# Optimization experiments

Hardware: AMD Instinct MI355X
Metric: run time of the kernel (lower is better)

Reference implementation:

```python
import jax, jax.numpy as jnp
import numpy as np

D_MODEL = 1024
N_HEADS = 16
D_K = D_MODEL // N_HEADS
B, S = 4, 2048


def setup_inputs() -> dict:
    key = jax.random.key(0)
    ks = jax.random.split(key, 5)
    scale = 1.0 / np.sqrt(D_MODEL)  # ~xavier scale for square matrices
    return {
        "Q": jax.random.normal(ks[0], (B, S, D_MODEL), dtype=jnp.float32),
        "length": jax.random.randint(ks[1], (B,), 1, S, dtype=jnp.int32),
        "Wq": jax.random.normal(ks[2], (D_MODEL, D_MODEL), dtype=jnp.float32) * scale,
        "bq": jnp.zeros((D_MODEL,), dtype=jnp.float32),
        "Wk": jax.random.normal(ks[3], (D_MODEL, D_MODEL), dtype=jnp.float32) * scale,
        "bk": jnp.zeros((D_MODEL,), dtype=jnp.float32),
        "Wv": jax.random.normal(ks[4], (D_MODEL, D_MODEL), dtype=jnp.float32) * scale,
        "bv": jnp.zeros((D_MODEL,), dtype=jnp.float32),
    }


def reference(Q, length, Wq, bq, Wk, bk, Wv, bv):
    b, s, d = Q.shape
    q_a = Q @ Wq + bq                                   # [b, s, d]
    # split heads: [b, h, s, d_k]
    q_s = q_a.reshape(b, s, N_HEADS, D_K).transpose(0, 2, 1, 3)
    k_s = (Q @ Wk + bk).reshape(b, s, N_HEADS, D_K).transpose(0, 2, 1, 3)
    v_s = (Q @ Wv + bv).reshape(b, s, N_HEADS, D_K).transpose(0, 2, 1, 3)

    # unnormalized exp attention with multiplicative key mask (faithful to source)
    scores = jnp.einsum("bhqd,bhkd->bhqk", q_s, k_s) / np.sqrt(D_K)
    scores = jnp.exp(scores)
    key_mask = (jnp.arange(s)[None, :] < length[:, None]).astype(scores.dtype)  # [b, k]
    scores = scores * key_mask[:, None, None, :]        # broadcast over heads, queries
    attn = scores / (jnp.sum(scores, axis=-1, keepdims=True) + 1e-8)
    context = jnp.einsum("bhqk,bhkd->bhqd", attn, v_s)
    context = context.transpose(0, 2, 1, 3).reshape(b, s, d)
    return context, q_a
```

## Files before the change

### kernel.cpp

```cpp
#include <hip/hip_runtime.h>

#define D_MODEL 1024
#define N_HEADS 16
#define D_KH    64
#define BATCH   4
#define SEQ     2048
#define M_TOTAL (BATCH*SEQ)

typedef __attribute__((ext_vector_type(8))) short short8;
typedef __attribute__((ext_vector_type(4))) float f32x4;
typedef __attribute__((ext_vector_type(4))) unsigned short u16x4;
typedef __attribute__((ext_vector_type(2))) unsigned int u32x2;

__device__ __forceinline__ unsigned short f2bf(float f) {
  union { float f; unsigned u; } v; v.f = f;
  unsigned r = v.u + 0x7FFFu + ((v.u >> 16) & 1u);
  return (unsigned short)(r >> 16);
}
__device__ __forceinline__ unsigned fbits(float f) {
  union { float f; unsigned u; } v; v.f = f; return v.u;
}

__global__ __launch_bounds__(256) void cvt_q(const float* __restrict__ Q,
                                             unsigned short* __restrict__ Qbf) {
  size_t i = (size_t)blockIdx.x * 256 + threadIdx.x;
  float4 v = ((const float4*)Q)[i];
  u16x4 o;
  o[0] = f2bf(v.x); o[1] = f2bf(v.y); o[2] = f2bf(v.z); o[3] = f2bf(v.w);
  ((u16x4*)Qbf)[i] = o;
}

__global__ __launch_bounds__(256) void cvt_wt(const float* __restrict__ Wq,
                                              const float* __restrict__ Wk,
                                              const float* __restrict__ Wv,
                                              unsigned short* __restrict__ WT) {
  const int z = blockIdx.z;
  const float* W = (z == 0) ? Wq : (z == 1) ? Wk : Wv;
  __shared__ float tile[32][33];
  const int k0 = blockIdx.y * 32, n0 = blockIdx.x * 32;
  const int tx = threadIdx.x & 31, ty = threadIdx.x >> 5;
  for (int i = 0; i < 4; ++i)
    tile[ty + i * 8][tx] = W[(size_t)(k0 + ty + i * 8) * D_MODEL + n0 + tx];
  __syncthreads();
  unsigned short* out = WT + (size_t)z * D_MODEL * D_MODEL;
  for (int i = 0; i < 4; ++i)
    out[(size_t)(n0 + ty + i * 8) * D_MODEL + k0 + tx] = f2bf(tile[tx][ty + i * 8]);
}

#define GQ_BM 128
#define GQ_BN 128
#define GQ_BK 64
#define GQ_NT (D_MODEL / GQ_BK)

__global__ __launch_bounds__(256, 2) void gemm_qkv(
    const unsigned short* __restrict__ Qbf,
    const unsigned short* __restrict__ WT,
    const float* __restrict__ bq_p, const float* __restrict__ bk_p,
    const float* __restrict__ bv_p,
    float* __restrict__ out_qa,
    unsigned short* __restrict__ kbf,
    unsigned short* __restrict__ vt) {
  const int f   = blockIdx.x;
  const int swz = (f & 7) * 192 + (f >> 3);
  const int mm  = swz / 24;
  const int nn  = swz % 24;
  const int m0  = mm * GQ_BM;
  const int n0g = nn * GQ_BN;
  const int z   = n0g >> 10;
  const int n0  = n0g & 1023;

  __shared__ unsigned short smA[2][GQ_BM * GQ_BK];
  __shared__ unsigned short smB[2][GQ_BN * GQ_BK];

  const int t    = threadIdx.x;
  const int lane = t & 63;
  const int w    = t >> 6;
  const int quad = lane >> 4;
  const int l16  = lane & 15;
  const int wr   = w >> 1, wc = w & 1;

  f32x4 acc[4][4];
  for (int i = 0; i < 4; ++i)
    for (int j = 0; j < 4; ++j) acc[i][j] = (f32x4){0.f, 0.f, 0.f, 0.f};

  auto stage = [&](int p, int kt) {
    #pragma unroll
    for (int r = 0; r < 4; ++r) {
      int o   = (r * 256 + t) * 8;
      int row = o >> 6;
      int col = (o & 63) ^ ((row & 7) << 3);
      const unsigned short* ga = Qbf + (size_t)(m0 + row)  * D_MODEL + kt * 64 + col;
      const unsigned short* gb = WT  + (size_t)(n0g + row) * D_MODEL + kt * 64 + col;
      __builtin_amdgcn_global_load_lds(
          (const __attribute__((address_space(1))) void*)ga,
          (__attribute__((address_space(3))) void*)&smA[p][o], 16, 0, 0);
      __builtin_amdgcn_global_load_lds(
          (const __attribute__((address_space(1))) void*)gb,
          (__attribute__((address_space(3))) void*)&smB[p][o], 16, 0, 0);
    }
  };

  stage(0, 0);
  stage(1, 1);
  asm volatile("s_waitcnt vmcnt(8)" ::: "memory");
  __builtin_amdgcn_s_barrier();
  asm volatile("" ::: "memory");

  for (int kt = 0; kt < GQ_NT; ++kt) {
    const int p = kt & 1;

    short8 af[4][2], bf[4][2];
    #pragma unroll
    for (int mi = 0; mi < 4; ++mi) {
      int row = wr * 64 + mi * 16 + l16;
      #pragma unroll
      for (int kk = 0; kk < 2; ++kk)
        af[mi][kk] = *(const short8*)
            &smA[p][(row * 64 + kk * 32 + quad * 8) ^ ((row & 7) << 3)];
    }
    #pragma unroll
    for (int ni = 0; ni < 4; ++ni) {
      int row = wc * 64 + ni * 16 + l16;
      #pragma unroll
      for (int kk = 0; kk < 2; ++kk)
        bf[ni][kk] = *(const short8*)
            &smB[p][(row * 64 + kk * 32 + quad * 8) ^ ((row & 7) << 3)];
    }

    __builtin_amdgcn_s_setprio(1);
    #pragma unroll
    for (int mi = 0; mi < 4; ++mi)
      #pragma unroll
      for (int ni = 0; ni < 4; ++ni) {
        acc[mi][ni] = __builtin_amdgcn_mfma_f32_16x16x32_bf16(
            af[mi][0], bf[ni][0], acc[mi][ni], 0, 0, 0);
        acc[mi][ni] = __builtin_amdgcn_mfma_f32_16x16x32_bf16(
            af[mi][1], bf[ni][1], acc[mi][ni], 0, 0, 0);
      }
    __builtin_amdgcn_s_setprio(0);

    __builtin_amdgcn_s_barrier();
    asm volatile("" ::: "memory");
    if (kt + 2 < GQ_NT) {
      stage(p, kt + 2);
      asm volatile("s_waitcnt vmcnt(8)" ::: "memory");
    } else {
      asm volatile("s_waitcnt vmcnt(0)" ::: "memory");
    }
    __builtin_amdgcn_s_barrier();
    asm volatile("" ::: "memory");
  }

  const float* bias = (z == 0) ? bq_p : (z == 1) ? bk_p : bv_p;
  if (z == 2) {
    for (int ni = 0; ni < 4; ++ni) {
      int n = n0 + wc * 64 + ni * 16 + l16;
      float bval = bias[n];
      int h = n >> 6, d = n & 63;
      for (int mi = 0; mi < 4; ++mi) {
        int m = m0 + wr * 64 + mi * 16 + quad * 4;
        int b = m >> 11, s = m & 2047;
        u16x4 o;
        for (int j = 0; j < 4; ++j) o[j] = f2bf(acc[mi][ni][j] + bval);
        *(u16x4*)&vt[(size_t)((b * 16 + h) * 64 + d) * SEQ + s] = o;
      }
    }
  } else {
    for (int ni = 0; ni < 4; ++ni) {
      int n = n0 + wc * 64 + ni * 16 + l16;
      float bval = bias[n];
      for (int mi = 0; mi < 4; ++mi) {
        int mbase = m0 + wr * 64 + mi * 16 + quad * 4;
        for (int j = 0; j < 4; ++j) {
          float v = acc[mi][ni][j] + bval;
          size_t idx = (size_t)(mbase + j) * D_MODEL + n;
          if (z == 0) out_qa[idx] = v;
          else        kbf[idx] = f2bf(v);
        }
      }
    }
  }
}

#define PST 72
#define QBLK 128

__global__ __launch_bounds__(256, 4) void attn(
    const float* __restrict__ qa,
    const unsigned short* __restrict__ kbf,
    const unsigned short* __restrict__ vt,
    const int* __restrict__ length,
    float* __restrict__ ctx) {
  const int flat = blockIdx.y * 16 + blockIdx.x;
  const int low = flat & 3;
  const int mid = (flat >> 2) & 15;
  const int hi  = flat >> 6;
  const int b  = (low + mid + (mid >> 2) + hi + (hi >> 2)) & 3;
  const int h  = mid;
  const int qt = hi;
  const int bh = b * 16 + h;
  const int len = length[b];

  const int t    = threadIdx.x;
  const int lane = t & 63;
  const int w    = t >> 6;
  const int quad = lane >> 4;
  const int l16  = lane & 15;
  const int r8   = t >> 3;
  const int c8   = (t & 7) * 8;

  __shared__ unsigned short sQ[QBLK * PST];
  __shared__ unsigned short sK[64 * PST];
  __shared__ unsigned short sVT[64 * PST];
  unsigned short* const sP = sQ;

  const float SCL = 0.125f * 1.44269504f;

  for (int half = 0; half < 4; ++half) {
    int r = r8 + half * 32;
    const float* src = qa + (size_t)(b * SEQ + qt * QBLK + r) * D_MODEL + h * D_KH + c8;
    float4 v0 = *(const float4*)src;
    float4 v1 = *(const float4*)(src + 4);
    short8 o;
    o[0] = (short)f2bf(v0.x * SCL); o[1] = (short)f2bf(v0.y * SCL);
    o[2] = (short)f2bf(v0.z * SCL); o[3] = (short)f2bf(v0.w * SCL);
    o[4] = (short)f2bf(v1.x * SCL); o[5] = (short)f2bf(v1.y * SCL);
    o[6] = (short)f2bf(v1.z * SCL); o[7] = (short)f2bf(v1.w * SCL);
    *(short8*)&sQ[r * PST + c8] = o;
  }
  __syncthreads();

  short8 qf00 = *(const short8*)&sQ[(w * 16 + l16) * PST + quad * 8];
  short8 qf01 = *(const short8*)&sQ[(w * 16 + l16) * PST + 32 + quad * 8];
  short8 qf10 = *(const short8*)&sQ[(64 + w * 16 + l16) * PST + quad * 8];
  short8 qf11 = *(const short8*)&sQ[(64 + w * 16 + l16) * PST + 32 + quad * 8];

  f32x4 acc0[4], acc1[4];
  for (int i = 0; i < 4; ++i) {
    acc0[i] = (f32x4){0.f, 0.f, 0.f, 0.f};
    acc1[i] = (f32x4){0.f, 0.f, 0.f, 0.f};
  }
  float den0 = 0.f, den1 = 0.f;

  const unsigned short* kbase_p = kbf + (size_t)b * SEQ * D_MODEL + h * D_KH;
  const unsigned short* vbase_p = vt + (size_t)bh * 64 * SEQ;

  const int nkt = (len + 63) >> 6;

  short8 rk[2], rv[2];
  for (int half = 0; half < 2; ++half) {
    int r = r8 + half * 32;
    rk[half] = *(const short8*)(kbase_p + (size_t)r * D_MODEL + c8);
    rv[half] = *(const short8*)(vbase_p + (size_t)r * SEQ + c8);
  }

  for (int kt = 0; kt < nkt; ++kt) {
    __syncthreads();
    for (int half = 0; half < 2; ++half) {
      int r = r8 + half * 32;
      *(short8*)&sK[r * PST + c8]  = rk[half];
      *(short8*)&sVT[r * PST + c8] = rv[half];
    }
    __syncthreads();

    if (kt + 1 < nkt) {
      for (int half = 0; half < 2; ++half) {
        int r = r8 + half * 32;
        rk[half] = *(const short8*)(kbase_p + (size_t)((kt + 1) * 64 + r) * D_MODEL + c8);
        rv[half] = *(const short8*)(vbase_p + (size_t)r * SEQ + (kt + 1) * 64 + c8);
      }
    }

    const bool full = ((kt + 1) << 6) <= len;

    for (int n = 0; n < 4; ++n) {
      short8 kf0 = *(const short8*)&sK[(n * 16 + l16) * PST + quad * 8];
      short8 kf1 = *(const short8*)&sK[(n * 16 + l16) * PST + 32 + quad * 8];
      f32x4 s0 = (f32x4){0.f, 0.f, 0.f, 0.f};
      s0 = __builtin_amdgcn_mfma_f32_16x16x32_bf16(kf0, qf00, s0, 0, 0, 0);
      s0 = __builtin_amdgcn_mfma_f32_16x16x32_bf16(kf1, qf01, s0, 0, 0, 0);
      f32x4 s1 = (f32x4){0.f, 0.f, 0.f, 0.f};
      s1 = __builtin_amdgcn_mfma_f32_16x16x32_bf16(kf0, qf10, s1, 0, 0, 0);
      s1 = __builtin_amdgcn_mfma_f32_16x16x32_bf16(kf1, qf11, s1, 0, 0, 0);

      float e0, e1, e2, e3, f0, f1, f2, f3;
      if (full) {
        e0 = exp2f(s0[0]); e1 = exp2f(s0[1]); e2 = exp2f(s0[2]); e3 = exp2f(s0[3]);
        f0 = exp2f(s1[0]); f1 = exp2f(s1[1]); f2 = exp2f(s1[2]); f3 = exp2f(s1[3]);
      } else {
        int kb = kt * 64 + n * 16 + quad * 4;
        e0 = (kb + 0 < len) ? exp2f(s0[0]) : 0.f;
        e1 = (kb + 1 < len) ? exp2f(s0[1]) : 0.f;
        e2 = (kb + 2 < len) ? exp2f(s0[2]) : 0.f;
        e3 = (kb + 3 < len) ? exp2f(s0[3]) : 0.f;
        f0 = (kb + 0 < len) ? exp2f(s1[0]) : 0.f;
        f1 = (kb + 1 < len) ? exp2f(s1[1]) : 0.f;
        f2 = (kb + 2 < len) ? exp2f(s1[2]) : 0.f;
        f3 = (kb + 3 < len) ? exp2f(s1[3]) : 0.f;
      }
      den0 += (e0 + e1) + (e2 + e3);
      den1 += (f0 + f1) + (f2 + f3);
      u32x2 pk;
      pk[0] = __builtin_amdgcn_perm(fbits(e1), fbits(e0), 0x07060302);
      pk[1] = __builtin_amdgcn_perm(fbits(e3), fbits(e2), 0x07060302);
      *(u32x2*)&sP[(w * 16 + l16) * PST + n * 16 + quad * 4] = pk;
      u32x2 pk1;
      pk1[0] = __builtin_amdgcn_perm(fbits(f1), fbits(f0), 0x07060302);
      pk1[1] = __builtin_amdgcn_perm(fbits(f3), fbits(f2), 0x07060302);
      *(u32x2*)&sP[(64 + w * 16 + l16) * PST + n * 16 + quad * 4] = pk1;
    }

    short8 pf00 = *(const short8*)&sP[(w * 16 + l16) * PST + quad * 8];
    short8 pf01 = *(const short8*)&sP[(w * 16 + l16) * PST + 32 + quad * 8];
    short8 pf10 = *(const short8*)&sP[(64 + w * 16 + l16) * PST + quad * 8];
    short8 pf11 = *(const short8*)&sP[(64 + w * 16 + l16) * PST + 32 + quad * 8];
    for (int n2 = 0; n2 < 4; ++n2) {
      short8 vf0 = *(const short8*)&sVT[(n2 * 16 + l16) * PST + quad * 8];
      short8 vf1 = *(const short8*)&sVT[(n2 * 16 + l16) * PST + 32 + quad * 8];
      acc0[n2] = __builtin_amdgcn_mfma_f32_16x16x32_bf16(vf0, pf00, acc0[n2], 0, 0, 0);
      acc0[n2] = __builtin_amdgcn_mfma_f32_16x16x32_bf16(vf1, pf01, acc0[n2], 0, 0, 0);
      acc1[n2] = __builtin_amdgcn_mfma_f32_16x16x32_bf16(vf0, pf10, acc1[n2], 0, 0, 0);
      acc1[n2] = __builtin_amdgcn_mfma_f32_16x16x32_bf16(vf1, pf11, acc1[n2], 0, 0, 0);
    }
  }

  den0 += __shfl_xor(den0, 16, 64);
  den0 += __shfl_xor(den0, 32, 64);
  den1 += __shfl_xor(den1, 16, 64);
  den1 += __shfl_xor(den1, 32, 64);
  float inv0 = 1.f / (den0 + 1e-8f);
  float inv1 = 1.f / (den1 + 1e-8f);

  {
    int q0 = qt * QBLK + w * 16 + l16;
    float* dst0 = ctx + (size_t)(b * SEQ + q0) * D_MODEL + h * D_KH;
    float* dst1 = dst0 + (size_t)64 * D_MODEL;
    for (int n2 = 0; n2 < 4; ++n2) {
      f32x4 o0 = acc0[n2];
      f32x4 o1 = acc1[n2];
      *(float4*)(dst0 + n2 * 16 + quad * 4) =
          make_float4(o0[0] * inv0, o0[1] * inv0, o0[2] * inv0, o0[3] * inv0);
      *(float4*)(dst1 + n2 * 16 + quad * 4) =
          make_float4(o1[0] * inv1, o1[1] * inv1, o1[2] * inv1, o1[3] * inv1);
    }
  }
}

extern "C" void kernel_launch(void* const* d_in, const int* in_sizes, int n_in,
                              void* d_out, int out_size, void* d_ws, size_t ws_size,
                              hipStream_t stream) {
  const float* Q      = (const float*)d_in[0];
  const int*   length = (const int*)d_in[1];
  const float* Wq     = (const float*)d_in[2];
  const float* bq     = (const float*)d_in[3];
  const float* Wk     = (const float*)d_in[4];
  const float* bk     = (const float*)d_in[5];
  const float* Wv     = (const float*)d_in[6];
  const float* bv     = (const float*)d_in[7];

  float* out_ctx = (float*)d_out;
  float* out_qa  = out_ctx + (size_t)M_TOTAL * D_MODEL;

  char* ws = (char*)d_ws;
  unsigned short* Qbf = (unsigned short*)ws;
  unsigned short* WT  = (unsigned short*)(ws + (size_t)16 * 1024 * 1024);
  unsigned short* Kbf = (unsigned short*)(ws + (size_t)22 * 1024 * 1024);
  unsigned short* Vt  = (unsigned short*)(ws + (size_t)38 * 1024 * 1024);

  hipLaunchKernelGGL(cvt_q, dim3((M_TOTAL * D_MODEL) / (256 * 4)), dim3(256), 0, stream,
                     Q, Qbf);
  hipLaunchKernelGGL(cvt_wt, dim3(32, 32, 3), dim3(256), 0, stream, Wq, Wk, Wv, WT);
  hipLaunchKernelGGL(gemm_qkv, dim3(64 * 24), dim3(256), 0, stream,
                     Qbf, WT, bq, bk, bv, out_qa, Kbf, Vt);
  hipLaunchKernelGGL(attn, dim3(SEQ / QBLK, BATCH * N_HEADS), dim3(256), 0, stream,
                     out_qa, Kbf, Vt, length, out_ctx);
}
```

Baseline: 243.5 us.

## Split attention key tiles across two wave sets and swizzle shared memory

The attention kernel now launches 512 threads per block. Two groups of four waves each process alternating 64-key tiles for the same 128 queries, and their partial accumulators and denominators are merged through shared memory at the end. The padded LDS layout (stride 72) is replaced by an XOR-swizzled 64-wide layout to avoid bank conflicts. The aim is more waves per block to hide latency and to shorten the serial key loop. In exchange it uses 64KB of LDS, which can lower the number of resident blocks per CU, and adds a reduction step.

```diff
diff --git a/kernel.cpp b/kernel.cpp
--- a/kernel.cpp
+++ b/kernel.cpp
@@ -19,6 +19,9 @@
 }
 __device__ __forceinline__ unsigned fbits(float f) {
   union { float f; unsigned u; } v; v.f = f; return v.u;
+}
+__device__ __forceinline__ int sw(int row, int col) {
+  return row * 64 + (col ^ ((row & 7) << 3));
 }
 
 __global__ __launch_bounds__(256) void cvt_q(const float* __restrict__ Q,
@@ -182,10 +185,9 @@
   }
 }
 
-#define PST 72
 #define QBLK 128
 
-__global__ __launch_bounds__(256, 4) void attn(
+__global__ __launch_bounds__(512, 4) void attn(
     const float* __restrict__ qa,
     const unsigned short* __restrict__ kbf,
     const unsigned short* __restrict__ vt,
@@ -203,22 +205,29 @@
 
   const int t    = threadIdx.x;
   const int lane = t & 63;
-  const int w    = t >> 6;
+  const int wv   = t >> 6;
+  const int set  = wv >> 2;
+  const int w2   = wv & 3;
   const int quad = lane >> 4;
   const int l16  = lane & 15;
-  const int r8   = t >> 3;
-  const int c8   = (t & 7) * 8;
-
-  __shared__ unsigned short sQ[QBLK * PST];
-  __shared__ unsigned short sK[64 * PST];
-  __shared__ unsigned short sVT[64 * PST];
-  unsigned short* const sP = sQ;
+  const int ts   = t & 255;
+  const int rs   = ts >> 3;
+  const int cs   = (ts & 7) * 8;
+
+  __shared__ unsigned char smem[65536];
+  unsigned short* sQP0 = (unsigned short*)smem;
+  unsigned short* sP1  = (unsigned short*)(smem + 16384);
+  unsigned short* sKs  = (unsigned short*)(smem + 32768 + set * 16384);
+  unsigned short* sVTs = sKs + 4096;
+  unsigned short* sPs  = set ? sP1 : sQP0;
+  float* sAcc = (float*)(smem + 32768);
+  float* sDen = (float*)(smem + 16384);
 
   const float SCL = 0.125f * 1.44269504f;
 
-  for (int half = 0; half < 4; ++half) {
-    int r = r8 + half * 32;
-    const float* src = qa + (size_t)(b * SEQ + qt * QBLK + r) * D_MODEL + h * D_KH + c8;
+  for (int half = 0; half < 2; ++half) {
+    int r = (t >> 3) + half * 64;
+    const float* src = qa + (size_t)(b * SEQ + qt * QBLK + r) * D_MODEL + h * D_KH + (t & 7) * 8;
     float4 v0 = *(const float4*)src;
     float4 v1 = *(const float4*)(src + 4);
     short8 o;
@@ -226,14 +235,16 @@
     o[2] = (short)f2bf(v0.z * SCL); o[3] = (short)f2bf(v0.w * SCL);
     o[4] = (short)f2bf(v1.x * SCL); o[5] = (short)f2bf(v1.y * SCL);
     o[6] = (short)f2bf(v1.z * SCL); o[7] = (short)f2bf(v1.w * SCL);
-    *(short8*)&sQ[r * PST + c8] = o;
+    *(short8*)&sQP0[sw(r, (t & 7) * 8)] = o;
   }
   __syncthreads();
 
-  short8 qf00 = *(const short8*)&sQ[(w * 16 + l16) * PST + quad * 8];
-  short8 qf01 = *(const short8*)&sQ[(w * 16 + l16) * PST + 32 + quad * 8];
-  short8 qf10 = *(const short8*)&sQ[(64 + w * 16 + l16) * PST + quad * 8];
-  short8 qf11 = *(const short8*)&sQ[(64 + w * 16 + l16) * PST + 32 + quad * 8];
+  const int qr0 = w2 * 16 + l16;
+  const int qr1 = 64 + qr0;
+  short8 qf00 = *(const short8*)&sQP0[sw(qr0, quad * 8)];
+  short8 qf01 = *(const short8*)&sQP0[sw(qr0, 32 + quad * 8)];
+  short8 qf10 = *(const short8*)&sQP0[sw(qr1, quad * 8)];
+  short8 qf11 = *(const short8*)&sQP0[sw(qr1, 32 + quad * 8)];
 
   f32x4 acc0[4], acc1[4];
   for (int i = 0; i < 4; ++i) {
@@ -245,82 +256,90 @@
   const unsigned short* kbase_p = kbf + (size_t)b * SEQ * D_MODEL + h * D_KH;
   const unsigned short* vbase_p = vt + (size_t)bh * 64 * SEQ;
 
-  const int nkt = (len + 63) >> 6;
+  const int nkt   = (len + 63) >> 6;
+  const int niter = (nkt + 1) >> 1;
 
   short8 rk[2], rv[2];
   for (int half = 0; half < 2; ++half) {
-    int r = r8 + half * 32;
-    rk[half] = *(const short8*)(kbase_p + (size_t)r * D_MODEL + c8);
-    rv[half] = *(const short8*)(vbase_p + (size_t)r * SEQ + c8);
-  }
-
-  for (int kt = 0; kt < nkt; ++kt) {
+    int r = rs + half * 32;
+    rk[half] = *(const short8*)(kbase_p + (size_t)(set * 64 + r) * D_MODEL + cs);
+    rv[half] = *(const short8*)(vbase_p + (size_t)r * SEQ + set * 64 + cs);
+  }
+
+  for (int i = 0; i < niter; ++i) {
+    const int kt = 2 * i + set;
+    const bool active = kt < nkt;
+
     __syncthreads();
-    for (int half = 0; half < 2; ++half) {
-      int r = r8 + half * 32;
-      *(short8*)&sK[r * PST + c8]  = rk[half];
-      *(short8*)&sVT[r * PST + c8] = rv[half];
+    if (active) {
+      for (int half = 0; half < 2; ++half) {
+        int r = rs + half * 32;
+        *(short8*)&sKs[sw(r, cs)]  = rk[half];
+        *(short8*)&sVTs[sw(r, cs)] = rv[half];
+      }
     }
     __syncthreads();
 
-    if (kt + 1 < nkt) {
+    if (kt + 2 < nkt) {
       for (int half = 0; half < 2; ++half) {
-        int r = r8 + half * 32;
-        rk[half] = *(const short8*)(kbase_p + (size_t)((kt + 1) * 64 + r) * D_MODEL + c8);
-        rv[half] = *(const short8*)(vbase_p + (size_t)r * SEQ + (kt + 1) * 64 + c8);
-      }
-    }
-
-    const bool full = ((kt + 1) << 6) <= len;
-
-    for (int n = 0; n < 4; ++n) {
-      short8 kf0 = *(const short8*)&sK[(n * 16 + l16) * PST + quad * 8];
-      short8 kf1 = *(const short8*)&sK[(n * 16 + l16) * PST + 32 + quad * 8];
-      f32x4 s0 = (f32x4){0.f, 0.f, 0.f, 0.f};
-      s0 = __builtin_amdgcn_mfma_f32_16x16x32_bf16(kf0, qf00, s0, 0, 0, 0);
-      s0 = __builtin_amdgcn_mfma_f32_16x16x32_bf16(kf1, qf01, s0, 0, 0, 0);
-      f32x4 s1 = (f32x4){0.f, 0.f, 0.f, 0.f};
-      s1 = __builtin_amdgcn_mfma_f32_16x16x32_bf16(kf0, qf10, s1, 0, 0, 0);
-      s1 = __builtin_amdgcn_mfma_f32_16x16x32_bf16(kf1, qf11, s1, 0, 0, 0);
-
-      float e0, e1, e2, e3, f0, f1, f2, f3;
-      if (full) {
-        e0 = exp2f(s0[0]); e1 = exp2f(s0[1]); e2 = exp2f(s0[2]); e3 = exp2f(s0[3]);
-        f0 = exp2f(s1[0]); f1 = exp2f(s1[1]); f2 = exp2f(s1[2]); f3 = exp2f(s1[3]);
-      } else {
-        int kb = kt * 64 + n * 16 + quad * 4;
-        e0 = (kb + 0 < len) ? exp2f(s0[0]) : 0.f;
-        e1 = (kb + 1 < len) ? exp2f(s0[1]) : 0.f;
-        e2 = (kb + 2 < len) ? exp2f(s0[2]) : 0.f;
-        e3 = (kb + 3 < len) ? exp2f(s0[3]) : 0.f;
-        f0 = (kb + 0 < len) ? exp2f(s1[0]) : 0.f;
-        f1 = (kb + 1 < len) ? exp2f(s1[1]) : 0.f;
-        f2 = (kb + 2 < len) ? exp2f(s1[2]) : 0.f;
-        f3 = (kb + 3 < len) ? exp2f(s1[3]) : 0.f;
-      }
-      den0 += (e0 + e1) + (e2 + e3);
-      den1 += (f0 + f1) + (f2 + f3);
-      u32x2 pk;
-      pk[0] = __builtin_amdgcn_perm(fbits(e1), fbits(e0), 0x07060302);
-      pk[1] = __builtin_amdgcn_perm(fbits(e3), fbits(e2), 0x07060302);
-      *(u32x2*)&sP[(w * 16 + l16) * PST + n * 16 + quad * 4] = pk;
-      u32x2 pk1;
-      pk1[0] = __builtin_amdgcn_perm(fbits(f1), fbits(f0), 0x07060302);
-      pk1[1] = __builtin_amdgcn_perm(fbits(f3), fbits(f2), 0x07060302);
-      *(u32x2*)&sP[(64 + w * 16 + l16) * PST + n * 16 + quad * 4] = pk1;
-    }
-
-    short8 pf00 = *(const short8*)&sP[(w * 16 + l16) * PST + quad * 8];
-    short8 pf01 = *(const short8*)&sP[(w * 16 + l16) * PST + 32 + quad * 8];
-    short8 pf10 = *(const short8*)&sP[(64 + w * 16 + l16) * PST + quad * 8];
-    short8 pf11 = *(const short8*)&sP[(64 + w * 16 + l16) * PST + 32 + quad * 8];
-    for (int n2 = 0; n2 < 4; ++n2) {
-      short8 vf0 = *(const short8*)&sVT[(n2 * 16 + l16) * PST + quad * 8];
-      short8 vf1 = *(const short8*)&sVT[(n2 * 16 + l16) * PST + 32 + quad * 8];
-      acc0[n2] = __builtin_amdgcn_mfma_f32_16x16x32_bf16(vf0, pf00, acc0[n2], 0, 0, 0);
-      acc0[n2] = __builtin_amdgcn_mfma_f32_16x16x32_bf16(vf1, pf01, acc0[n2], 0, 0, 0);
-      acc1[n2] = __builtin_amdgcn_mfma_f32_16x16x32_bf16(vf0, pf10, acc1[n2], 0, 0, 0);
-      acc1[n2] = __builtin_amdgcn_mfma_f32_16x16x32_bf16(vf1, pf11, acc1[n2], 0, 0, 0);
+        int r = rs + half * 32;
+        rk[half] = *(const short8*)(kbase_p + (size_t)((kt + 2) * 64 + r) * D_MODEL + cs);
+        rv[half] = *(const short8*)(vbase_p + (size_t)r * SEQ + (kt + 2) * 64 + cs);
+      }
+    }
+
+    if (active) {
+      const bool full = ((kt + 1) << 6) <= len;
+
+      for (int n = 0; n < 4; ++n) {
+        short8 kf0 = *(const short8*)&sKs[sw(n * 16 + l16, quad * 8)];
+        short8 kf1 = *(const short8*)&sKs[sw(n * 16 + l16, 32 + quad * 8)];
+        f32x4 s0 = (f32x4){0.f, 0.f, 0.f, 0.f};
+        s0 = __builtin_amdgcn_mfma_f32_16x16x32_bf16(kf0, qf00, s0, 0, 0, 0);
+        s0 = __builtin_amdgcn_mfma_f32_16x16x32_bf16(kf1, qf01, s0, 0, 0, 0);
+        f32x4 s1 = (f32x4){0.f, 0.f, 0.f, 0.f};
+        s1 = __builtin_amdgcn_mfma_f32_16x16x32_bf16(kf0, qf10, s1, 0, 0, 0);
+        s1 = __builtin_amdgcn_mfma_f32_16x16x32_bf16(kf1, qf11, s1, 0, 0, 0);
+
+        float e0, e1, e2, e3, f0, f1, f2, f3;
+        if (full) {
+          e0 = exp2f(s0[0]); e1 = exp2f(s0[1]); e2 = exp2f(s0[2]); e3 = exp2f(s0[3]);
+          f0 = exp2f(s1[0]); f1 = exp2f(s1[1]); f2 = exp2f(s1[2]); f3 = exp2f(s1[3]);
+        } else {
+          int kb = kt * 64 + n * 16 + quad * 4;
+          e0 = (kb + 0 < len) ? exp2f(s0[0]) : 0.f;
+          e1 = (kb + 1 < len) ? exp2f(s0[1]) : 0.f;
+          e2 = (kb + 2 < len) ? exp2f(s0[2]) : 0.f;
+          e3 = (kb + 3 < len) ? exp2f(s0[3]) : 0.f;
+          f0 = (kb + 0 < len) ? exp2f(s1[0]) : 0.f;
+          f1 = (kb + 1 < len) ? exp2f(s1[1]) : 0.f;
+          f2 = (kb + 2 < len) ? exp2f(s1[2]) : 0.f;
+          f3 = (kb + 3 < len) ? exp2f(s1[3]) : 0.f;
+        }
+        den0 += (e0 + e1) + (e2 + e3);
+        den1 += (f0 + f1) + (f2 + f3);
+        u32x2 pk;
+        pk[0] = __builtin_amdgcn_perm(fbits(e1), fbits(e0), 0x07060302);
+        pk[1] = __builtin_amdgcn_perm(fbits(e3), fbits(e2), 0x07060302);
+        *(u32x2*)&sPs[sw(qr0, n * 16 + quad * 4)] = pk;
+        u32x2 pk1;
+        pk1[0] = __builtin_amdgcn_perm(fbits(f1), fbits(f0), 0x07060302);
+        pk1[1] = __builtin_amdgcn_perm(fbits(f3), fbits(f2), 0x07060302);
+        *(u32x2*)&sPs[sw(qr1, n * 16 + quad * 4)] = pk1;
+      }
+
+      short8 pf00 = *(const short8*)&sPs[sw(qr0, quad * 8)];
+      short8 pf01 = *(const short8*)&sPs[sw(qr0, 32 + quad * 8)];
+      short8 pf10 = *(const short8*)&sPs[sw(qr1, quad * 8)];
+      short8 pf11 = *(const short8*)&sPs[sw(qr1, 32 + quad * 8)];
+      for (int n2 = 0; n2 < 4; ++n2) {
+        short8 vf0 = *(const short8*)&sVTs[sw(n2 * 16 + l16, quad * 8)];
+        short8 vf1 = *(const short8*)&sVTs[sw(n2 * 16 + l16, 32 + quad * 8)];
+        acc0[n2] = __builtin_amdgcn_mfma_f32_16x16x32_bf16(vf0, pf00, acc0[n2], 0, 0, 0);
+        acc0[n2] = __builtin_amdgcn_mfma_f32_16x16x32_bf16(vf1, pf01, acc0[n2], 0, 0, 0);
+        acc1[n2] = __builtin_amdgcn_mfma_f32_16x16x32_bf16(vf0, pf10, acc1[n2], 0, 0, 0);
+        acc1[n2] = __builtin_amdgcn_mfma_f32_16x16x32_bf16(vf1, pf11, acc1[n2], 0, 0, 0);
+      }
     }
   }
 
@@ -328,20 +347,34 @@
   den0 += __shfl_xor(den0, 32, 64);
   den1 += __shfl_xor(den1, 16, 64);
   den1 += __shfl_xor(den1, 32, 64);
-  float inv0 = 1.f / (den0 + 1e-8f);
-  float inv1 = 1.f / (den1 + 1e-8f);
-
-  {
-    int q0 = qt * QBLK + w * 16 + l16;
-    float* dst0 = ctx + (size_t)(b * SEQ + q0) * D_MODEL + h * D_KH;
-    float* dst1 = dst0 + (size_t)64 * D_MODEL;
+
+  __syncthreads();
+  if (set == 1) {
+    #pragma unroll
     for (int n2 = 0; n2 < 4; ++n2) {
-      f32x4 o0 = acc0[n2];
-      f32x4 o1 = acc1[n2];
-      *(float4*)(dst0 + n2 * 16 + quad * 4) =
-          make_float4(o0[0] * inv0, o0[1] * inv0, o0[2] * inv0, o0[3] * inv0);
-      *(float4*)(dst1 + n2 * 16 + quad * 4) =
-          make_float4(o1[0] * inv1, o1[1] * inv1, o1[2] * inv1, o1[3] * inv1);
+      int col = n2 * 16 + quad * 4;
+      *(f32x4*)&sAcc[qr0 * 64 + (col ^ ((qr0 & 7) << 2))] = acc0[n2];
+      *(f32x4*)&sAcc[qr1 * 64 + (col ^ ((qr1 & 7) << 2))] = acc1[n2];
+    }
+    if (quad == 0) { sDen[qr0] = den0; sDen[qr1] = den1; }
+  }
+  __syncthreads();
+  if (set == 0) {
+    float inv0 = 1.f / (den0 + sDen[qr0] + 1e-8f);
+    float inv1 = 1.f / (den1 + sDen[qr1] + 1e-8f);
+    float* dst0 = ctx + (size_t)(b * SEQ + qt * QBLK + qr0) * D_MODEL + h * D_KH;
+    float* dst1 = ctx + (size_t)(b * SEQ + qt * QBLK + qr1) * D_MODEL + h * D_KH;
+    #pragma unroll
+    for (int n2 = 0; n2 < 4; ++n2) {
+      int col = n2 * 16 + quad * 4;
+      f32x4 p0 = *(const f32x4*)&sAcc[qr0 * 64 + (col ^ ((qr0 & 7) << 2))];
+      f32x4 p1 = *(const f32x4*)&sAcc[qr1 * 64 + (col ^ ((qr1 & 7) << 2))];
+      *(float4*)(dst0 + col) = make_float4(
+          (acc0[n2][0] + p0[0]) * inv0, (acc0[n2][1] + p0[1]) * inv0,
+          (acc0[n2][2] + p0[2]) * inv0, (acc0[n2][3] + p0[3]) * inv0);
+      *(float4*)(dst1 + col) = make_float4(
+          (acc1[n2][0] + p1[0]) * inv1, (acc1[n2][1] + p1[1]) * inv1,
+          (acc1[n2][2] + p1[2]) * inv1, (acc1[n2][3] + p1[3]) * inv1);
     }
   }
 }
@@ -372,6 +405,6 @@
   hipLaunchKernelGGL(cvt_wt, dim3(32, 32, 3), dim3(256), 0, stream, Wq, Wk, Wv, WT);
   hipLaunchKernelGGL(gemm_qkv, dim3(64 * 24), dim3(256), 0, stream,
                      Qbf, WT, bq, bk, bv, out_qa, Kbf, Vt);
-  hipLaunchKernelGGL(attn, dim3(SEQ / QBLK, BATCH * N_HEADS), dim3(256), 0, stream,
+  hipLaunchKernelGGL(attn, dim3(SEQ / QBLK, BATCH * N_HEADS), dim3(512), 0, stream,
                      out_qa, Kbf, Vt, length, out_ctx);
 }
```

After: 286.7 us. 17.7% more time.

## Load K/V MFMA fragments directly from global memory, drop LDS staging and barriers

Applied to the files above, without the earlier changes.

The attention kernel no longer stages K and V^T tiles in shared memory with double-buffered register prefetch and two barriers per tile. Each wave now loads its MFMA K and V fragments straight from global memory, which removes the per-tile __syncthreads and LDS traffic. The Q/P shared buffer switches from padded rows to an XOR-swizzled 64-wide layout to avoid bank conflicts. In exchange, every wave reloads the same K/V data from global/L2 (four times redundant per block) with no software prefetch, so exposed load latency may dominate.

```diff
diff --git a/kernel.cpp b/kernel.cpp
--- a/kernel.cpp
+++ b/kernel.cpp
@@ -19,6 +19,9 @@
 }
 __device__ __forceinline__ unsigned fbits(float f) {
   union { float f; unsigned u; } v; v.f = f; return v.u;
+}
+__device__ __forceinline__ int sw(int row, int col) {
+  return row * 64 + (col ^ ((row & 7) << 3));
 }
 
 __global__ __launch_bounds__(256) void cvt_q(const float* __restrict__ Q,
@@ -182,7 +185,6 @@
   }
 }
 
-#define PST 72
 #define QBLK 128
 
 __global__ __launch_bounds__(256, 4) void attn(
@@ -209,10 +211,8 @@
   const int r8   = t >> 3;
   const int c8   = (t & 7) * 8;
 
-  __shared__ unsigned short sQ[QBLK * PST];
-  __shared__ unsigned short sK[64 * PST];
-  __shared__ unsigned short sVT[64 * PST];
-  unsigned short* const sP = sQ;
+  __shared__ unsigned short sQP[QBLK * 64];
+  unsigned short* const sP = sQP;
 
   const float SCL = 0.125f * 1.44269504f;
 
@@ -226,14 +226,16 @@
     o[2] = (short)f2bf(v0.z * SCL); o[3] = (short)f2bf(v0.w * SCL);
     o[4] = (short)f2bf(v1.x * SCL); o[5] = (short)f2bf(v1.y * SCL);
     o[6] = (short)f2bf(v1.z * SCL); o[7] = (short)f2bf(v1.w * SCL);
-    *(short8*)&sQ[r * PST + c8] = o;
+    *(short8*)&sQP[sw(r, c8)] = o;
   }
   __syncthreads();
 
-  short8 qf00 = *(const short8*)&sQ[(w * 16 + l16) * PST + quad * 8];
-  short8 qf01 = *(const short8*)&sQ[(w * 16 + l16) * PST + 32 + quad * 8];
-  short8 qf10 = *(const short8*)&sQ[(64 + w * 16 + l16) * PST + quad * 8];
-  short8 qf11 = *(const short8*)&sQ[(64 + w * 16 + l16) * PST + 32 + quad * 8];
+  const int qr0 = w * 16 + l16;
+  const int qr1 = 64 + qr0;
+  short8 qf00 = *(const short8*)&sQP[sw(qr0, quad * 8)];
+  short8 qf01 = *(const short8*)&sQP[sw(qr0, 32 + quad * 8)];
+  short8 qf10 = *(const short8*)&sQP[sw(qr1, quad * 8)];
+  short8 qf11 = *(const short8*)&sQP[sw(qr1, 32 + quad * 8)];
 
   f32x4 acc0[4], acc1[4];
   for (int i = 0; i < 4; ++i) {
@@ -242,46 +244,32 @@
   }
   float den0 = 0.f, den1 = 0.f;
 
-  const unsigned short* kbase_p = kbf + (size_t)b * SEQ * D_MODEL + h * D_KH;
-  const unsigned short* vbase_p = vt + (size_t)bh * 64 * SEQ;
+  const unsigned short* kfp = kbf + (size_t)b * SEQ * D_MODEL + h * D_KH
+                              + (size_t)l16 * D_MODEL + quad * 8;
+  const unsigned short* vfp = vt + (size_t)bh * 64 * SEQ
+                              + (size_t)l16 * SEQ + quad * 8;
 
   const int nkt = (len + 63) >> 6;
 
-  short8 rk[2], rv[2];
-  for (int half = 0; half < 2; ++half) {
-    int r = r8 + half * 32;
-    rk[half] = *(const short8*)(kbase_p + (size_t)r * D_MODEL + c8);
-    rv[half] = *(const short8*)(vbase_p + (size_t)r * SEQ + c8);
-  }
-
   for (int kt = 0; kt < nkt; ++kt) {
-    __syncthreads();
-    for (int half = 0; half < 2; ++half) {
-      int r = r8 + half * 32;
-      *(short8*)&sK[r * PST + c8]  = rk[half];
-      *(short8*)&sVT[r * PST + c8] = rv[half];
-    }
-    __syncthreads();
-
-    if (kt + 1 < nkt) {
-      for (int half = 0; half < 2; ++half) {
-        int r = r8 + half * 32;
-        rk[half] = *(const short8*)(kbase_p + (size_t)((kt + 1) * 64 + r) * D_MODEL + c8);
-        rv[half] = *(const short8*)(vbase_p + (size_t)r * SEQ + (kt + 1) * 64 + c8);
-      }
-    }
-
     const bool full = ((kt + 1) << 6) <= len;
 
+    short8 kf[4][2];
+    #pragma unroll
     for (int n = 0; n < 4; ++n) {
-      short8 kf0 = *(const short8*)&sK[(n * 16 + l16) * PST + quad * 8];
-      short8 kf1 = *(const short8*)&sK[(n * 16 + l16) * PST + 32 + quad * 8];
+      const unsigned short* kp = kfp + (size_t)(kt * 64 + n * 16) * D_MODEL;
+      kf[n][0] = *(const short8*)kp;
+      kf[n][1] = *(const short8*)(kp + 32);
+    }
+
+    #pragma unroll
+    for (int n = 0; n < 4; ++n) {
       f32x4 s0 = (f32x4){0.f, 0.f, 0.f, 0.f};
-      s0 = __builtin_amdgcn_mfma_f32_16x16x32_bf16(kf0, qf00, s0, 0, 0, 0);
-      s0 = __builtin_amdgcn_mfma_f32_16x16x32_bf16(kf1, qf01, s0, 0, 0, 0);
+      s0 = __builtin_amdgcn_mfma_f32_16x16x32_bf16(kf[n][0], qf00, s0, 0, 0, 0);
+      s0 = __builtin_amdgcn_mfma_f32_16x16x32_bf16(kf[n][1], qf01, s0, 0, 0, 0);
       f32x4 s1 = (f32x4){0.f, 0.f, 0.f, 0.f};
-      s1 = __builtin_amdgcn_mfma_f32_16x16x32_bf16(kf0, qf10, s1, 0, 0, 0);
-      s1 = __builtin_amdgcn_mfma_f32_16x16x32_bf16(kf1, qf11, s1, 0, 0, 0);
+      s1 = __builtin_amdgcn_mfma_f32_16x16x32_bf16(kf[n][0], qf10, s1, 0, 0, 0);
+      s1 = __builtin_amdgcn_mfma_f32_16x16x32_bf16(kf[n][1], qf11, s1, 0, 0, 0);
 
       float e0, e1, e2, e3, f0, f1, f2, f3;
       if (full) {
@@ -303,24 +291,31 @@
       u32x2 pk;
       pk[0] = __builtin_amdgcn_perm(fbits(e1), fbits(e0), 0x07060302);
       pk[1] = __builtin_amdgcn_perm(fbits(e3), fbits(e2), 0x07060302);
-      *(u32x2*)&sP[(w * 16 + l16) * PST + n * 16 + quad * 4] = pk;
+      *(u32x2*)&sP[sw(qr0, n * 16 + quad * 4)] = pk;
       u32x2 pk1;
       pk1[0] = __builtin_amdgcn_perm(fbits(f1), fbits(f0), 0x07060302);
       pk1[1] = __builtin_amdgcn_perm(fbits(f3), fbits(f2), 0x07060302);
-      *(u32x2*)&sP[(64 + w * 16 + l16) * PST + n * 16 + quad * 4] = pk1;
-    }
-
-    short8 pf00 = *(const short8*)&sP[(w * 16 + l16) * PST + quad * 8];
-    short8 pf01 = *(const short8*)&sP[(w * 16 + l16) * PST + 32 + quad * 8];
-    short8 pf10 = *(const short8*)&sP[(64 + w * 16 + l16) * PST + quad * 8];
-    short8 pf11 = *(const short8*)&sP[(64 + w * 16 + l16) * PST + 32 + quad * 8];
+      *(u32x2*)&sP[sw(qr1, n * 16 + quad * 4)] = pk1;
+    }
+
+    short8 vf[4][2];
+    #pragma unroll
     for (int n2 = 0; n2 < 4; ++n2) {
-      short8 vf0 = *(const short8*)&sVT[(n2 * 16 + l16) * PST + quad * 8];
-      short8 vf1 = *(const short8*)&sVT[(n2 * 16 + l16) * PST + 32 + quad * 8];
-      acc0[n2] = __builtin_amdgcn_mfma_f32_16x16x32_bf16(vf0, pf00, acc0[n2], 0, 0, 0);
-      acc0[n2] = __builtin_amdgcn_mfma_f32_16x16x32_bf16(vf1, pf01, acc0[n2], 0, 0, 0);
-      acc1[n2] = __builtin_amdgcn_mfma_f32_16x16x32_bf16(vf0, pf10, acc1[n2], 0, 0, 0);
-      acc1[n2] = __builtin_amdgcn_mfma_f32_16x16x32_bf16(vf1, pf11, acc1[n2], 0, 0, 0);
+      const unsigned short* vp = vfp + (size_t)(n2 * 16) * SEQ + kt * 64;
+      vf[n2][0] = *(const short8*)vp;
+      vf[n2][1] = *(const short8*)(vp + 32);
+    }
+
+    short8 pf00 = *(const short8*)&sP[sw(qr0, quad * 8)];
+    short8 pf01 = *(const short8*)&sP[sw(qr0, 32 + quad * 8)];
+    short8 pf10 = *(const short8*)&sP[sw(qr1, quad * 8)];
+    short8 pf11 = *(const short8*)&sP[sw(qr1, 32 + quad * 8)];
+    #pragma unroll
+    for (int n2 = 0; n2 < 4; ++n2) {
+      acc0[n2] = __builtin_amdgcn_mfma_f32_16x16x32_bf16(vf[n2][0], pf00, acc0[n2], 0, 0, 0);
+      acc0[n2] = __builtin_amdgcn_mfma_f32_16x16x32_bf16(vf[n2][1], pf01, acc0[n2], 0, 0, 0);
+      acc1[n2] = __builtin_amdgcn_mfma_f32_16x16x32_bf16(vf[n2][0], pf10, acc1[n2], 0, 0, 0);
+      acc1[n2] = __builtin_amdgcn_mfma_f32_16x16x32_bf16(vf[n2][1], pf11, acc1[n2], 0, 0, 0);
     }
   }
 
```

Result: slower. 306.7 us (+26.0%).
